# Kernel tuning notes

Hardware: AMD Instinct MI355X
Metric: run time of the kernel (lower is better)

The kernel has to match this reference:

```python
import jax, jax.numpy as jnp
import numpy as np

EPS = 1e-08

def log_g(x):
    return jnp.log(jnp.tanh(x) + EPS)

def parallel_scan(log_coeffs, log_values):
    # log_coeffs: [B, L, H], log_values: [B, L+1, H]
    a_star = jnp.pad(jnp.cumsum(log_coeffs, axis=1), ((0, 0), (1, 0), (0, 0)))
    log_h0_plus_b_star = jax.lax.cumlogsumexp(log_values - a_star, axis=1)
    log_h = a_star + log_h0_plus_b_star
    return jnp.exp(log_h)[:, 1:, :]

def setup_inputs() -> dict:
    key = jax.random.key(0)
    B, L, I, H, O = 16, 4096, 64, 512, 1
    ks = jax.random.split(key, 8)
    s_i = 1.0 / np.sqrt(I)
    s_h = 1.0 / np.sqrt(H)
    return {
        "x": jax.random.normal(ks[0], (B, L, I), dtype=jnp.float32),
        "Wz0": jax.random.uniform(ks[1], (I, H), jnp.float32, -s_i, s_i),
        "bz0": jnp.zeros((H,), jnp.float32),
        "Wh0": jax.random.uniform(ks[2], (I, H), jnp.float32, -s_i, s_i),
        "bh0": jnp.zeros((H,), jnp.float32),
        "Wz1": jax.random.uniform(ks[3], (H, H), jnp.float32, -s_h, s_h),
        "bz1": jnp.zeros((H,), jnp.float32),
        "Wh1": jax.random.uniform(ks[4], (H, H), jnp.float32, -s_h, s_h),
        "bh1": jnp.zeros((H,), jnp.float32),
        "Wf": jax.random.uniform(ks[5], (H, O), jnp.float32, -s_h, s_h),
        "bf": jnp.zeros((O,), jnp.float32),
    }

def min_gru_layer(inp, Wz, bz, Wh, bh):
    B, L, _ = inp.shape
    H = Wz.shape[1]
    k = jax.nn.sigmoid(inp @ Wz + bz)          # [B, L, H]
    log_z = -jax.nn.softplus(-k)               # (faithful: softplus of sigmoid output)
    log_coeffs = -jax.nn.softplus(k)
    log_h0 = jnp.full((B, 1, H), jnp.log(EPS), dtype=inp.dtype)  # log_g(zeros)
    log_h_wavy = log_g(jax.nn.sigmoid(inp @ Wh + bh))
    log_values = jnp.concatenate([log_h0, log_z + log_h_wavy], axis=1)  # [B, L+1, H]
    return parallel_scan(log_coeffs, log_values)

def reference(x, Wz0, bz0, Wh0, bh0, Wz1, bz1, Wh1, bh1, Wf, bf):
    h = min_gru_layer(x, Wz0, bz0, Wh0, bh0)
    h = min_gru_layer(h, Wz1, bz1, Wh1, bh1)
    return h[:, -1, :] @ Wf + bf  # [B, output_size]
```

## Files before the change

### kernel.cpp

```cpp
#include <hip/hip_runtime.h>
#include <hip/hip_fp16.h>

#define EPSF 1e-8f

typedef _Float16 half8 __attribute__((ext_vector_type(8)));
typedef float f32x4 __attribute__((ext_vector_type(4)));


__device__ __forceinline__ float fast_rcp(float x) {
    return __builtin_amdgcn_rcpf(x);
}
__device__ __forceinline__ void gate_transform(float pz, float ph, float& a, float& b) {
    float ez = __expf(-pz);
    float k  = fast_rcp(1.0f + ez);
    float ek = __expf(-k);
    float z  = fast_rcp(1.0f + ek);
    a = ek * z;
    float es = __expf(-ph);
    float s  = fast_rcp(1.0f + es);
    float e2 = __expf(-2.0f * s);
    float hw = (1.0f - e2) * fast_rcp(1.0f + e2) + EPSF;
    b = z * hw;
}

__device__ __forceinline__ void gload16(const void* g, void* l) {
    __builtin_amdgcn_global_load_lds(
        (const __attribute__((address_space(1))) unsigned int*)g,
        (__attribute__((address_space(3))) unsigned int*)l, 16, 0, 0);
}

__device__ __forceinline__ void qscan(int q, float pA, float pB,
                                      float& fA, float& fB, float& prA, float& prB)
{
    float oA = __shfl_xor(pA, 16, 64), oB = __shfl_xor(pB, 16, 64);
    float eA = (q & 1) ? oA : pA, eB = (q & 1) ? oB : pB;
    float lA = (q & 1) ? pA : oA, lB = (q & 1) ? pB : oB;
    float p2A = eA * lA;
    float p2B = fmaf(lA, eB, lB);
    float o2A = __shfl_xor(p2A, 32, 64), o2B = __shfl_xor(p2B, 32, 64);
    float loA = (q & 2) ? o2A : p2A, loB = (q & 2) ? o2B : p2B;
    float hiA = (q & 2) ? p2A : o2A, hiB = (q & 2) ? p2B : o2B;
    fA = loA * hiA;
    fB = fmaf(hiA, loB, hiB);
    prA = (q & 2) ? o2A : 1.0f;
    prB = (q & 2) ? o2B : 0.0f;
    if (q & 1) { prB = fmaf(oA, prB, oB); prA *= oA; }
}

__global__ __launch_bounds__(256) void k1s(
    const float* __restrict__ x,
    const float* __restrict__ Wz0, const float* __restrict__ Wh0,
    const float* __restrict__ Wz1, const float* __restrict__ Wh1,
    const float* __restrict__ bz, const float* __restrict__ bh,
    const float* __restrict__ bf,
    __half* __restrict__ Wtz1, __half* __restrict__ Wth1,
    __half* __restrict__ h0red, float* __restrict__ out)
{
    __shared__ char smem1[49408];
    __half* As = (__half*)smem1;
    __half* Bs = As + 128 * 64;
    float (*t)[65] = (float(*)[65])(smem1 + 32768);
    float* carray = (float*)(smem1 + 16384);
    __half* h0s = (__half*)smem1;
    const int tid = threadIdx.x;
    const int wave = tid >> 6, lane = tid & 63;
    const int q = lane >> 4, l16 = lane & 15;
    const int wm = wave >> 1, wn = wave & 1;

    const int bx = blockIdx.x, by = blockIdx.y;
    const int Lb = bx + 8 * by;
    const int n0 = bx * 64;
    const float* xsrc = x + (size_t)by * 262144 + 253952;

    if (Lb == 0 && tid < 16) out[tid] = bf[0];

    {
        const int r8 = lane >> 3, ch = lane & 7;
#pragma unroll
        for (int i = 0; i < 4; ++i) {
            const int reg = wave * 4 + i;
            const int row = reg * 8 + r8;
            const int c0 = (ch ^ (row & 7)) * 8;
            float4 v0 = *(const float4*)(xsrc + row * 64 + c0);
            float4 v1 = *(const float4*)(xsrc + row * 64 + c0 + 4);
            __half2* dst = (__half2*)((char*)As + reg * 1024 + lane * 16);
            dst[0] = __floats2half2_rn(v0.x, v0.y);
            dst[1] = __floats2half2_rn(v0.z, v0.w);
            dst[2] = __floats2half2_rn(v1.x, v1.y);
            dst[3] = __floats2half2_rn(v1.z, v1.w);
        }
    }

    const int r = tid >> 4, c4 = (tid & 15) * 4;
    {
        const int mat = Lb >> 6, ti = Lb & 63;
        const int n0t = (ti & 7) * 64, k0t = (ti >> 3) * 64;
        const float* W = mat ? Wh1 : Wz1;
        __half* Wt = mat ? Wth1 : Wtz1;
#pragma unroll
        for (int rr = 0; rr < 64; rr += 16)
            *(float4*)&t[rr + r][c4] = *(const float4*)&W[(size_t)(k0t + rr + r) * 512 + n0t + c4];
        __syncthreads();
#pragma unroll
        for (int rr = 0; rr < 64; rr += 16) {
            const int row = rr + r;
            __half2 h01 = __floats2half2_rn(t[c4 + 0][row], t[c4 + 1][row]);
            __half2 h23 = __floats2half2_rn(t[c4 + 2][row], t[c4 + 3][row]);
            *(__half2*)&Wt[(size_t)(n0t + row) * 512 + k0t + c4] = h01;
            *(__half2*)&Wt[(size_t)(n0t + row) * 512 + k0t + c4 + 2] = h23;
        }
    }
    {
        const int n = tid & 63, cw = (tid >> 6) * 2;
#pragma unroll
        for (int mat = 0; mat < 2; ++mat) {
            const float* W = mat ? Wh0 : Wz0;
            __syncthreads();
#pragma unroll
            for (int rr = 0; rr < 64; rr += 16)
                *(float4*)&t[rr + r][c4] = *(const float4*)&W[(size_t)(rr + r) * 512 + n0 + c4];
            __syncthreads();
#pragma unroll
            for (int cc = 0; cc < 2; ++cc) {
                const int chunk = cw + cc;
                half8 hv;
#pragma unroll
                for (int j = 0; j < 8; ++j) hv[j] = (_Float16)t[chunk * 8 + j][n];
                *(half8*)&Bs[(mat * 64 + n) * 64 + ((chunk ^ (n & 7)) << 3)] = hv;
            }
        }
    }
    __syncthreads();

    f32x4 accz[4][2], acch[4][2];
#pragma unroll
    for (int mi = 0; mi < 4; ++mi)
#pragma unroll
        for (int ni = 0; ni < 2; ++ni) {
            accz[mi][ni] = (f32x4){0.f, 0.f, 0.f, 0.f};
            acch[mi][ni] = (f32x4){0.f, 0.f, 0.f, 0.f};
        }

#pragma unroll
    for (int s = 0; s < 2; ++s) {
        half8 af[4];
#pragma unroll
        for (int mi = 0; mi < 4; ++mi) {
            const int row = wm * 64 + mi * 16 + l16;
            const int pc = (s * 4 + q) ^ (row & 7);
            af[mi] = *(const half8*)&As[row * 64 + pc * 8];
        }
#pragma unroll
        for (int ni = 0; ni < 2; ++ni) {
            const int rn = wn * 32 + ni * 16 + l16;
            const int pc = (s * 4 + q) ^ (rn & 7);
            half8 bzf = *(const half8*)&Bs[rn * 64 + pc * 8];
            half8 bhf = *(const half8*)&Bs[(64 + rn) * 64 + pc * 8];
#pragma unroll
            for (int mi = 0; mi < 4; ++mi) {
                accz[mi][ni] = __builtin_amdgcn_mfma_f32_16x16x32_f16(af[mi], bzf, accz[mi][ni], 0, 0, 0);
                acch[mi][ni] = __builtin_amdgcn_mfma_f32_16x16x32_f16(af[mi], bhf, acch[mi][ni], 0, 0, 0);
            }
        }
    }

    float rB[2];
    if (wm == 0) {
#pragma unroll
        for (int ni = 0; ni < 2; ++ni) {
            const int col = n0 + wn * 32 + ni * 16 + l16;
            const float bzv = bz[col], bhv = bh[col];
            float runA = 1.f, runB = 0.f;
#pragma unroll
            for (int mi = 0; mi < 4; ++mi) {
                float av[4], bv[4], pA = 1.f, pB = 0.f;
#pragma unroll
                for (int j = 0; j < 4; ++j) {
                    gate_transform(accz[mi][ni][j] + bzv, acch[mi][ni][j] + bhv, av[j], bv[j]);
                    pB = fmaf(av[j], pB, bv[j]); pA *= av[j];
                }
                float fA, fB, prA, prB;
                qscan(q, pA, pB, fA, fB, prA, prB);
                runB = fmaf(fA, runB, fB); runA *= fA;
            }
            rB[ni] = runB;
        }
    }
    __syncthreads();
    if (wm == 0 && q == 0) {
#pragma unroll
        for (int ni = 0; ni < 2; ++ni)
            carray[wn * 32 + ni * 16 + l16] = rB[ni];
    }
    __syncthreads();
    if (wm == 1) {
#pragma unroll
        for (int ni = 0; ni < 2; ++ni) {
            const int colloc = wn * 32 + ni * 16 + l16;
            const int col = n0 + colloc;
            const float bzv = bz[col], bhv = bh[col];
            float H = carray[colloc];
#pragma unroll
            for (int mi = 0; mi < 4; ++mi) {
                float av[4], bv[4], pA = 1.f, pB = 0.f;
#pragma unroll
                for (int j = 0; j < 4; ++j) {
                    gate_transform(accz[mi][ni][j] + bzv, acch[mi][ni][j] + bhv, av[j], bv[j]);
                    pB = fmaf(av[j], pB, bv[j]); pA *= av[j];
                }
                float fA, fB, prA, prB;
                qscan(q, pA, pB, fA, fB, prA, prB);
                float Hl = fmaf(prA, H, prB);
                const int rloc = mi * 16 + q * 4;
#pragma unroll
                for (int j = 0; j < 4; ++j) {
                    Hl = fmaf(av[j], Hl, bv[j]);
                    h0s[(rloc + j) * 68 + colloc] = (__half)Hl;
                }
                H = fmaf(fA, H, fB);
            }
        }
    }
    __syncthreads();
    {
        const int row = tid >> 2, cpart = tid & 3;
        const __half* srcp = h0s + row * 68 + cpart * 16;
        __half* dstp = h0red + (size_t)(by * 64 + row) * 512 + n0 + cpart * 16;
        *(uint4*)dstp = *(const uint4*)srcp;
        *(uint4*)(dstp + 8) = *(const uint4*)(srcp + 8);
    }
}

__global__ __launch_bounds__(256, 2) void k4_l1(
    const __half* __restrict__ h0red,
    const __half* __restrict__ Wtz, const __half* __restrict__ Wth,
    const float* __restrict__ bz, const float* __restrict__ bh,
    const float* __restrict__ Wf, float* __restrict__ out)
{
    __shared__ char smem4[2][24576];
    const int tid = threadIdx.x;
    const int wave = tid >> 6, lane = tid & 63;
    const int q = lane >> 4, l16 = lane & 15;
    const int wm = wave >> 1, wn = wave & 1;

    const int bx = blockIdx.x, by = blockIdx.y;
    const int m0 = by * 128, n0 = bx * 128;

    const int r4 = lane >> 2, ch = lane & 3;

    const __half* aSrc[2]; int aDst[2];
#pragma unroll
    for (int i = 0; i < 2; ++i) {
        const int reg = wave * 2 + i;
        const int row = reg * 16 + r4;
        const int pc = ch ^ ((row >> 1) & 3);
        aSrc[i] = h0red + (size_t)(m0 + row) * 512 + pc * 8;
        aDst[i] = reg * 1024;
    }
    const __half* bSrc[4]; int bDst[4];
#pragma unroll
    for (int i = 0; i < 4; ++i) {
        const int reg = wave * 4 + i;
        const int row = reg * 16 + r4;
        const int pc = ch ^ ((row >> 1) & 3);
        bSrc[i] = ((row < 128) ? (Wtz + (size_t)(n0 + row) * 512)
                               : (Wth + (size_t)(n0 + row - 128) * 512)) + pc * 8;
        bDst[i] = 8192 + reg * 1024;
    }
    int aOff[4], bOff[4];
#pragma unroll
    for (int mi = 0; mi < 4; ++mi) {
        const int row = wm * 64 + mi * 16 + l16;
        aOff[mi] = row * 64 + ((q ^ ((row >> 1) & 3)) << 4);
    }
#pragma unroll
    for (int ni = 0; ni < 4; ++ni) {
        const int rn = wn * 64 + ni * 16 + l16;
        bOff[ni] = 8192 + rn * 64 + ((q ^ ((rn >> 1) & 3)) << 4);
    }

    f32x4 accz[4][4], acch[4][4];
#pragma unroll
    for (int mi = 0; mi < 4; ++mi)
#pragma unroll
        for (int ni = 0; ni < 4; ++ni) {
            accz[mi][ni] = (f32x4){0.f, 0.f, 0.f, 0.f};
            acch[mi][ni] = (f32x4){0.f, 0.f, 0.f, 0.f};
        }

    auto stage = [&](int c, int t) {
#pragma unroll
        for (int i = 0; i < 2; ++i)
            gload16(aSrc[i] + t * 32, smem4[c] + aDst[i]);
#pragma unroll
        for (int i = 0; i < 4; ++i)
            gload16(bSrc[i] + t * 32, smem4[c] + bDst[i]);
    };
    auto compute = [&](int c) {
        half8 af[4];
#pragma unroll
        for (int mi = 0; mi < 4; ++mi)
            af[mi] = *(const half8*)(smem4[c] + aOff[mi]);
        __builtin_amdgcn_s_setprio(1);
#pragma unroll
        for (int ni = 0; ni < 4; ++ni) {
            half8 bzf = *(const half8*)(smem4[c] + bOff[ni]);
            half8 bhf = *(const half8*)(smem4[c] + 8192 + bOff[ni]);
#pragma unroll
            for (int mi = 0; mi < 4; ++mi) {
                accz[mi][ni] = __builtin_amdgcn_mfma_f32_16x16x32_f16(af[mi], bzf, accz[mi][ni], 0, 0, 0);
                acch[mi][ni] = __builtin_amdgcn_mfma_f32_16x16x32_f16(af[mi], bhf, acch[mi][ni], 0, 0, 0);
            }
        }
        __builtin_amdgcn_s_setprio(0);
    };

    stage(0, 0);
#pragma unroll
    for (int t = 0; t < 15; ++t) {
        const int c = t & 1;
        stage(c ^ 1, t + 1);
        asm volatile("s_waitcnt vmcnt(6)" ::: "memory");
        __builtin_amdgcn_s_barrier();
        compute(c);
        __builtin_amdgcn_s_barrier();
    }
    asm volatile("s_waitcnt vmcnt(0)" ::: "memory");
    __builtin_amdgcn_s_barrier();
    compute(1);

    const int batch = by * 2 + wm;
    float part = 0.f;
#pragma unroll
    for (int ni = 0; ni < 4; ++ni) {
        const int col = n0 + wn * 64 + ni * 16 + l16;
        const float bzv = bz[col], bhv = bh[col];
        float fullA = 1.f, fullB = 0.f;
#pragma unroll
        for (int mi = 0; mi < 4; ++mi) {
            float pA = 1.f, pB = 0.f;
#pragma unroll
            for (int j = 0; j < 4; ++j) {
                float a, b;
                gate_transform(accz[mi][ni][j] + bzv, acch[mi][ni][j] + bhv, a, b);
                pB = fmaf(a, pB, b); pA *= a;
            }
            float fA, fB, prA, prB;
            qscan(q, pA, pB, fA, fB, prA, prB);
            fullB = fmaf(fA, fullB, fB); fullA *= fA;
        }
        if (q == 0) part = fmaf(fullB, Wf[col], part);
    }
#pragma unroll
    for (int off = 32; off; off >>= 1) part += __shfl_down(part, off, 64);
    if (lane == 0) atomicAdd(&out[batch], part);
}

extern "C" void kernel_launch(void* const* d_in, const int* in_sizes, int n_in,
                              void* d_out, int out_size, void* d_ws, size_t ws_size,
                              hipStream_t stream)
{
    const float* x   = (const float*)d_in[0];
    const float* Wz0 = (const float*)d_in[1];
    const float* bz0 = (const float*)d_in[2];
    const float* Wh0 = (const float*)d_in[3];
    const float* bh0 = (const float*)d_in[4];
    const float* Wz1 = (const float*)d_in[5];
    const float* bz1 = (const float*)d_in[6];
    const float* Wh1 = (const float*)d_in[7];
    const float* bh1 = (const float*)d_in[8];
    const float* Wf  = (const float*)d_in[9];
    const float* bf  = (const float*)d_in[10];
    float* out = (float*)d_out;

    char* ws = (char*)d_ws;
    __half* h0red = (__half*)ws;
    __half* Wtz1  = (__half*)(ws + (1024 << 10));
    __half* Wth1  = Wtz1 + 262144;

    k1s<<<dim3(8, 16), 256, 0, stream>>>(x, Wz0, Wh0, Wz1, Wh1, bz0, bh0, bf,
                                         Wtz1, Wth1, h0red, out);
    k4_l1<<<dim3(4, 8), 256, 0, stream>>>(h0red, Wtz1, Wth1, bz1, bh1, Wf, out);
}
```

Baseline: 32.31 us.

## Fuse both layer kernels into one launch with a global atomic barrier

Merges the layer-0 kernel and the layer-1 GEMM/scan kernel into a single 128-block launch. After writing its layer-0 hidden states, each block bumps a global counter. The first 32 blocks spin until all 128 have arrived, then run the layer-1 work. This removes one kernel launch gap but adds a memset before the launch, spin-wait latency, and reliance on all 128 blocks being co-resident so the barrier cannot deadlock.

Measured after the change: 42.62 us. 31.9% more time.

```diff
diff --git a/kernel.cpp b/kernel.cpp
--- a/kernel.cpp
+++ b/kernel.cpp
@@ -47,313 +47,320 @@
     if (q & 1) { prB = fmaf(oA, prB, oB); prA *= oA; }
 }
 
-__global__ __launch_bounds__(256) void k1s(
+__global__ __launch_bounds__(256) void kfused(
     const float* __restrict__ x,
     const float* __restrict__ Wz0, const float* __restrict__ Wh0,
     const float* __restrict__ Wz1, const float* __restrict__ Wh1,
-    const float* __restrict__ bz, const float* __restrict__ bh,
-    const float* __restrict__ bf,
+    const float* __restrict__ bz0, const float* __restrict__ bh0,
+    const float* __restrict__ bz1, const float* __restrict__ bh1,
+    const float* __restrict__ Wf, const float* __restrict__ bf,
     __half* __restrict__ Wtz1, __half* __restrict__ Wth1,
-    __half* __restrict__ h0red, float* __restrict__ out)
+    __half* __restrict__ h0red, unsigned int* __restrict__ cnt,
+    float* __restrict__ out)
 {
-    __shared__ char smem1[49408];
-    __half* As = (__half*)smem1;
-    __half* Bs = As + 128 * 64;
-    float (*t)[65] = (float(*)[65])(smem1 + 32768);
-    float* carray = (float*)(smem1 + 16384);
-    __half* h0s = (__half*)smem1;
+    __shared__ char smem[49408];
     const int tid = threadIdx.x;
     const int wave = tid >> 6, lane = tid & 63;
     const int q = lane >> 4, l16 = lane & 15;
     const int wm = wave >> 1, wn = wave & 1;
-
-    const int bx = blockIdx.x, by = blockIdx.y;
-    const int Lb = bx + 8 * by;
-    const int n0 = bx * 64;
-    const float* xsrc = x + (size_t)by * 262144 + 253952;
-
-    if (Lb == 0 && tid < 16) out[tid] = bf[0];
+    const int Lb = blockIdx.x;
 
     {
-        const int r8 = lane >> 3, ch = lane & 7;
+        __half* As = (__half*)smem;
+        __half* Bs = As + 128 * 64;
+        float (*t)[65] = (float(*)[65])(smem + 32768);
+        float* carray = (float*)(smem + 16384);
+        __half* h0s = (__half*)smem;
+
+        const int bx = Lb & 7, by = Lb >> 3;
+        const int n0 = bx * 64;
+        const float* xsrc = x + (size_t)by * 262144 + 253952;
+
+        if (Lb == 0 && tid < 16) out[tid] = bf[0];
+
+        {
+            const int r8 = lane >> 3, ch = lane & 7;
+#pragma unroll
+            for (int i = 0; i < 4; ++i) {
+                const int reg = wave * 4 + i;
+                const int row = reg * 8 + r8;
+                const int c0 = (ch ^ (row & 7)) * 8;
+                float4 v0 = *(const float4*)(xsrc + row * 64 + c0);
+                float4 v1 = *(const float4*)(xsrc + row * 64 + c0 + 4);
+                __half2* dst = (__half2*)((char*)As + reg * 1024 + lane * 16);
+                dst[0] = __floats2half2_rn(v0.x, v0.y);
+                dst[1] = __floats2half2_rn(v0.z, v0.w);
+                dst[2] = __floats2half2_rn(v1.x, v1.y);
+                dst[3] = __floats2half2_rn(v1.z, v1.w);
+            }
+        }
+
+        const int r = tid >> 4, c4 = (tid & 15) * 4;
+        {
+            const int mat = Lb >> 6, ti = Lb & 63;
+            const int n0t = (ti & 7) * 64, k0t = (ti >> 3) * 64;
+            const float* W = mat ? Wh1 : Wz1;
+            __half* Wt = mat ? Wth1 : Wtz1;
+#pragma unroll
+            for (int rr = 0; rr < 64; rr += 16)
+                *(float4*)&t[rr + r][c4] = *(const float4*)&W[(size_t)(k0t + rr + r) * 512 + n0t + c4];
+            __syncthreads();
+#pragma unroll
+            for (int rr = 0; rr < 64; rr += 16) {
+                const int row = rr + r;
+                __half2 h01 = __floats2half2_rn(t[c4 + 0][row], t[c4 + 1][row]);
+                __half2 h23 = __floats2half2_rn(t[c4 + 2][row], t[c4 + 3][row]);
+                *(__half2*)&Wt[(size_t)(n0t + row) * 512 + k0t + c4] = h01;
+                *(__half2*)&Wt[(size_t)(n0t + row) * 512 + k0t + c4 + 2] = h23;
+            }
+        }
+        {
+            const int n = tid & 63, cw = (tid >> 6) * 2;
+#pragma unroll
+            for (int mat = 0; mat < 2; ++mat) {
+                const float* W = mat ? Wh0 : Wz0;
+                __syncthreads();
+#pragma unroll
+                for (int rr = 0; rr < 64; rr += 16)
+                    *(float4*)&t[rr + r][c4] = *(const float4*)&W[(size_t)(rr + r) * 512 + n0 + c4];
+                __syncthreads();
+#pragma unroll
+                for (int cc = 0; cc < 2; ++cc) {
+                    const int chunk = cw + cc;
+                    half8 hv;
+#pragma unroll
+                    for (int j = 0; j < 8; ++j) hv[j] = (_Float16)t[chunk * 8 + j][n];
+                    *(half8*)&Bs[(mat * 64 + n) * 64 + ((chunk ^ (n & 7)) << 3)] = hv;
+                }
+            }
+        }
+        __syncthreads();
+
+        f32x4 accz[4][2], acch[4][2];
+#pragma unroll
+        for (int mi = 0; mi < 4; ++mi)
+#pragma unroll
+            for (int ni = 0; ni < 2; ++ni) {
+                accz[mi][ni] = (f32x4){0.f, 0.f, 0.f, 0.f};
+                acch[mi][ni] = (f32x4){0.f, 0.f, 0.f, 0.f};
+            }
+
+#pragma unroll
+        for (int s = 0; s < 2; ++s) {
+            half8 af[4];
+#pragma unroll
+            for (int mi = 0; mi < 4; ++mi) {
+                const int row = wm * 64 + mi * 16 + l16;
+                const int pc = (s * 4 + q) ^ (row & 7);
+                af[mi] = *(const half8*)&As[row * 64 + pc * 8];
+            }
+#pragma unroll
+            for (int ni = 0; ni < 2; ++ni) {
+                const int rn = wn * 32 + ni * 16 + l16;
+                const int pc = (s * 4 + q) ^ (rn & 7);
+                half8 bzf = *(const half8*)&Bs[rn * 64 + pc * 8];
+                half8 bhf = *(const half8*)&Bs[(64 + rn) * 64 + pc * 8];
+#pragma unroll
+                for (int mi = 0; mi < 4; ++mi) {
+                    accz[mi][ni] = __builtin_amdgcn_mfma_f32_16x16x32_f16(af[mi], bzf, accz[mi][ni], 0, 0, 0);
+                    acch[mi][ni] = __builtin_amdgcn_mfma_f32_16x16x32_f16(af[mi], bhf, acch[mi][ni], 0, 0, 0);
+                }
+            }
+        }
+
+        float rB[2];
+        if (wm == 0) {
+#pragma unroll
+            for (int ni = 0; ni < 2; ++ni) {
+                const int col = n0 + wn * 32 + ni * 16 + l16;
+                const float bzv = bz0[col], bhv = bh0[col];
+                float runA = 1.f, runB = 0.f;
+#pragma unroll
+                for (int mi = 0; mi < 4; ++mi) {
+                    float av[4], bv[4], pA = 1.f, pB = 0.f;
+#pragma unroll
+                    for (int j = 0; j < 4; ++j) {
+                        gate_transform(accz[mi][ni][j] + bzv, acch[mi][ni][j] + bhv, av[j], bv[j]);
+                        pB = fmaf(av[j], pB, bv[j]); pA *= av[j];
+                    }
+                    float fA, fB, prA, prB;
+                    qscan(q, pA, pB, fA, fB, prA, prB);
+                    runB = fmaf(fA, runB, fB); runA *= fA;
+                }
+                rB[ni] = runB;
+            }
+        }
+        __syncthreads();
+        if (wm == 0 && q == 0) {
+#pragma unroll
+            for (int ni = 0; ni < 2; ++ni)
+                carray[wn * 32 + ni * 16 + l16] = rB[ni];
+        }
+        __syncthreads();
+        if (wm == 1) {
+#pragma unroll
+            for (int ni = 0; ni < 2; ++ni) {
+                const int colloc = wn * 32 + ni * 16 + l16;
+                const int col = n0 + colloc;
+                const float bzv = bz0[col], bhv = bh0[col];
+                float H = carray[colloc];
+#pragma unroll
+                for (int mi = 0; mi < 4; ++mi) {
+                    float av[4], bv[4], pA = 1.f, pB = 0.f;
+#pragma unroll
+                    for (int j = 0; j < 4; ++j) {
+                        gate_transform(accz[mi][ni][j] + bzv, acch[mi][ni][j] + bhv, av[j], bv[j]);
+                        pB = fmaf(av[j], pB, bv[j]); pA *= av[j];
+                    }
+                    float fA, fB, prA, prB;
+                    qscan(q, pA, pB, fA, fB, prA, prB);
+                    float Hl = fmaf(prA, H, prB);
+                    const int rloc = mi * 16 + q * 4;
+#pragma unroll
+                    for (int j = 0; j < 4; ++j) {
+                        Hl = fmaf(av[j], Hl, bv[j]);
+                        h0s[(rloc + j) * 68 + colloc] = (__half)Hl;
+                    }
+                    H = fmaf(fA, H, fB);
+                }
+            }
+        }
+        __syncthreads();
+        {
+            const int row = tid >> 2, cpart = tid & 3;
+            const __half* srcp = h0s + row * 68 + cpart * 16;
+            __half* dstp = h0red + (size_t)(by * 64 + row) * 512 + n0 + cpart * 16;
+            *(uint4*)dstp = *(const uint4*)srcp;
+            *(uint4*)(dstp + 8) = *(const uint4*)(srcp + 8);
+        }
+    }
+
+    __syncthreads();
+    if (tid == 0) {
+        __threadfence();
+        atomicAdd(cnt, 1u);
+    }
+    if (Lb >= 32) return;
+    if (tid == 0) {
+        while (__hip_atomic_load(cnt, __ATOMIC_RELAXED, __HIP_MEMORY_SCOPE_AGENT) < 128u)
+            __builtin_amdgcn_s_sleep(2);
+    }
+    __syncthreads();
+    __threadfence();
+
+    {
+        char* smem4 = smem;
+        const int bx = Lb & 3, by = Lb >> 2;
+        const int m0 = by * 128, n0 = bx * 128;
+        const int r4 = lane >> 2, ch = lane & 3;
+
+        const __half* aSrc[2]; int aDst[2];
+#pragma unroll
+        for (int i = 0; i < 2; ++i) {
+            const int reg = wave * 2 + i;
+            const int row = reg * 16 + r4;
+            const int pc = ch ^ ((row >> 1) & 3);
+            aSrc[i] = h0red + (size_t)(m0 + row) * 512 + pc * 8;
+            aDst[i] = reg * 1024;
+        }
+        const __half* bSrc[4]; int bDst[4];
 #pragma unroll
         for (int i = 0; i < 4; ++i) {
             const int reg = wave * 4 + i;
-            const int row = reg * 8 + r8;
-            const int c0 = (ch ^ (row & 7)) * 8;
-            float4 v0 = *(const float4*)(xsrc + row * 64 + c0);
-            float4 v1 = *(const float4*)(xsrc + row * 64 + c0 + 4);
-            __half2* dst = (__half2*)((char*)As + reg * 1024 + lane * 16);
-            dst[0] = __floats2half2_rn(v0.x, v0.y);
-            dst[1] = __floats2half2_rn(v0.z, v0.w);
-            dst[2] = __floats2half2_rn(v1.x, v1.y);
-            dst[3] = __floats2half2_rn(v1.z, v1.w);
-        }
-    }
-
-    const int r = tid >> 4, c4 = (tid & 15) * 4;
-    {
-        const int mat = Lb >> 6, ti = Lb & 63;
-        const int n0t = (ti & 7) * 64, k0t = (ti >> 3) * 64;
-        const float* W = mat ? Wh1 : Wz1;
-        __half* Wt = mat ? Wth1 : Wtz1;
-#pragma unroll
-        for (int rr = 0; rr < 64; rr += 16)
-            *(float4*)&t[rr + r][c4] = *(const float4*)&W[(size_t)(k0t + rr + r) * 512 + n0t + c4];
-        __syncthreads();
-#pragma unroll
-        for (int rr = 0; rr < 64; rr += 16) {
-            const int row = rr + r;
-            __half2 h01 = __floats2half2_rn(t[c4 + 0][row], t[c4 + 1][row]);
-            __half2 h23 = __floats2half2_rn(t[c4 + 2][row], t[c4 + 3][row]);
-            *(__half2*)&Wt[(size_t)(n0t + row) * 512 + k0t + c4] = h01;
-            *(__half2*)&Wt[(size_t)(n0t + row) * 512 + k0t + c4 + 2] = h23;
-        }
-    }
-    {
-        const int n = tid & 63, cw = (tid >> 6) * 2;
-#pragma unroll
-        for (int mat = 0; mat < 2; ++mat) {
-            const float* W = mat ? Wh0 : Wz0;
-            __syncthreads();
-#pragma unroll
-            for (int rr = 0; rr < 64; rr += 16)
-                *(float4*)&t[rr + r][c4] = *(const float4*)&W[(size_t)(rr + r) * 512 + n0 + c4];
-            __syncthreads();
-#pragma unroll
-            for (int cc = 0; cc < 2; ++cc) {
-                const int chunk = cw + cc;
-                half8 hv;
-#pragma unroll
-                for (int j = 0; j < 8; ++j) hv[j] = (_Float16)t[chunk * 8 + j][n];
-                *(half8*)&Bs[(mat * 64 + n) * 64 + ((chunk ^ (n & 7)) << 3)] = hv;
-            }
-        }
-    }
-    __syncthreads();
-
-    f32x4 accz[4][2], acch[4][2];
-#pragma unroll
-    for (int mi = 0; mi < 4; ++mi)
-#pragma unroll
-        for (int ni = 0; ni < 2; ++ni) {
-            accz[mi][ni] = (f32x4){0.f, 0.f, 0.f, 0.f};
-            acch[mi][ni] = (f32x4){0.f, 0.f, 0.f, 0.f};
-        }
-
-#pragma unroll
-    for (int s = 0; s < 2; ++s) {
-        half8 af[4];
+            const int row = reg * 16 + r4;
+            const int pc = ch ^ ((row >> 1) & 3);
+            bSrc[i] = ((row < 128) ? (Wtz1 + (size_t)(n0 + row) * 512)
+                                   : (Wth1 + (size_t)(n0 + row - 128) * 512)) + pc * 8;
+            bDst[i] = 8192 + reg * 1024;
+        }
+        int aOff[4], bOff[4];
 #pragma unroll
         for (int mi = 0; mi < 4; ++mi) {
             const int row = wm * 64 + mi * 16 + l16;
-            const int pc = (s * 4 + q) ^ (row & 7);
-            af[mi] = *(const half8*)&As[row * 64 + pc * 8];
-        }
-#pragma unroll
-        for (int ni = 0; ni < 2; ++ni) {
-            const int rn = wn * 32 + ni * 16 + l16;
-            const int pc = (s * 4 + q) ^ (rn & 7);
-            half8 bzf = *(const half8*)&Bs[rn * 64 + pc * 8];
-            half8 bhf = *(const half8*)&Bs[(64 + rn) * 64 + pc * 8];
+            aOff[mi] = row * 64 + ((q ^ ((row >> 1) & 3)) << 4);
+        }
+#pragma unroll
+        for (int ni = 0; ni < 4; ++ni) {
+            const int rn = wn * 64 + ni * 16 + l16;
+            bOff[ni] = 8192 + rn * 64 + ((q ^ ((rn >> 1) & 3)) << 4);
+        }
+
+        f32x4 accz[4][4], acch[4][4];
+#pragma unroll
+        for (int mi = 0; mi < 4; ++mi)
+#pragma unroll
+            for (int ni = 0; ni < 4; ++ni) {
+                accz[mi][ni] = (f32x4){0.f, 0.f, 0.f, 0.f};
+                acch[mi][ni] = (f32x4){0.f, 0.f, 0.f, 0.f};
+            }
+
+        auto stage = [&](int c, int t) {
+#pragma unroll
+            for (int i = 0; i < 2; ++i)
+                gload16(aSrc[i] + t * 32, smem4 + c * 24576 + aDst[i]);
+#pragma unroll
+            for (int i = 0; i < 4; ++i)
+                gload16(bSrc[i] + t * 32, smem4 + c * 24576 + bDst[i]);
+        };
+        auto compute = [&](int c) {
+            half8 af[4];
+#pragma unroll
+            for (int mi = 0; mi < 4; ++mi)
+                af[mi] = *(const half8*)(smem4 + c * 24576 + aOff[mi]);
+            __builtin_amdgcn_s_setprio(1);
+#pragma unroll
+            for (int ni = 0; ni < 4; ++ni) {
+                half8 bzf = *(const half8*)(smem4 + c * 24576 + bOff[ni]);
+                half8 bhf = *(const half8*)(smem4 + c * 24576 + 8192 + bOff[ni]);
+#pragma unroll
+                for (int mi = 0; mi < 4; ++mi) {
+                    accz[mi][ni] = __builtin_amdgcn_mfma_f32_16x16x32_f16(af[mi], bzf, accz[mi][ni], 0, 0, 0);
+                    acch[mi][ni] = __builtin_amdgcn_mfma_f32_16x16x32_f16(af[mi], bhf, acch[mi][ni], 0, 0, 0);
+                }
+            }
+            __builtin_amdgcn_s_setprio(0);
+        };
+
+        stage(0, 0);
+#pragma unroll
+        for (int t = 0; t < 15; ++t) {
+            const int c = t & 1;
+            stage(c ^ 1, t + 1);
+            asm volatile("s_waitcnt vmcnt(6)" ::: "memory");
+            __builtin_amdgcn_s_barrier();
+            compute(c);
+            __builtin_amdgcn_s_barrier();
+        }
+        asm volatile("s_waitcnt vmcnt(0)" ::: "memory");
+        __builtin_amdgcn_s_barrier();
+        compute(1);
+
+        const int batch = by * 2 + wm;
+        float part = 0.f;
+#pragma unroll
+        for (int ni = 0; ni < 4; ++ni) {
+            const int col = n0 + wn * 64 + ni * 16 + l16;
+            const float bzv = bz1[col], bhv = bh1[col];
+            float fullA = 1.f, fullB = 0.f;
 #pragma unroll
             for (int mi = 0; mi < 4; ++mi) {
-                accz[mi][ni] = __builtin_amdgcn_mfma_f32_16x16x32_f16(af[mi], bzf, accz[mi][ni], 0, 0, 0);
-                acch[mi][ni] = __builtin_amdgcn_mfma_f32_16x16x32_f16(af[mi], bhf, acch[mi][ni], 0, 0, 0);
-            }
-        }
-    }
-
-    float rB[2];
-    if (wm == 0) {
-#pragma unroll
-        for (int ni = 0; ni < 2; ++ni) {
-            const int col = n0 + wn * 32 + ni * 16 + l16;
-            const float bzv = bz[col], bhv = bh[col];
-            float runA = 1.f, runB = 0.f;
-#pragma unroll
-            for (int mi = 0; mi < 4; ++mi) {
-                float av[4], bv[4], pA = 1.f, pB = 0.f;
+                float pA = 1.f, pB = 0.f;
 #pragma unroll
                 for (int j = 0; j < 4; ++j) {
-                    gate_transform(accz[mi][ni][j] + bzv, acch[mi][ni][j] + bhv, av[j], bv[j]);
-                    pB = fmaf(av[j], pB, bv[j]); pA *= av[j];
+                    float a, b;
+                    gate_transform(accz[mi][ni][j] + bzv, acch[mi][ni][j] + bhv, a, b);
+                    pB = fmaf(a, pB, b); pA *= a;
                 }
                 float fA, fB, prA, prB;
                 qscan(q, pA, pB, fA, fB, prA, prB);
-                runB = fmaf(fA, runB, fB); runA *= fA;
-            }
-            rB[ni] = runB;
-        }
+                fullB = fmaf(fA, fullB, fB); fullA *= fA;
+            }
+            if (q == 0) part = fmaf(fullB, Wf[col], part);
+        }
+#pragma unroll
+        for (int off = 32; off; off >>= 1) part += __shfl_down(part, off, 64);
+        if (lane == 0) atomicAdd(&out[batch], part);
     }
-    __syncthreads();
-    if (wm == 0 && q == 0) {
-#pragma unroll
-        for (int ni = 0; ni < 2; ++ni)
-            carray[wn * 32 + ni * 16 + l16] = rB[ni];
-    }
-    __syncthreads();
-    if (wm == 1) {
-#pragma unroll
-        for (int ni = 0; ni < 2; ++ni) {
-            const int colloc = wn * 32 + ni * 16 + l16;
-            const int col = n0 + colloc;
-            const float bzv = bz[col], bhv = bh[col];
-            float H = carray[colloc];
-#pragma unroll
-            for (int mi = 0; mi < 4; ++mi) {
-                float av[4], bv[4], pA = 1.f, pB = 0.f;
-#pragma unroll
-                for (int j = 0; j < 4; ++j) {
-                    gate_transform(accz[mi][ni][j] + bzv, acch[mi][ni][j] + bhv, av[j], bv[j]);
-                    pB = fmaf(av[j], pB, bv[j]); pA *= av[j];
-                }
-                float fA, fB, prA, prB;
-                qscan(q, pA, pB, fA, fB, prA, prB);
-                float Hl = fmaf(prA, H, prB);
-                const int rloc = mi * 16 + q * 4;
-#pragma unroll
-                for (int j = 0; j < 4; ++j) {
-                    Hl = fmaf(av[j], Hl, bv[j]);
-                    h0s[(rloc + j) * 68 + colloc] = (__half)Hl;
-                }
-                H = fmaf(fA, H, fB);
-            }
-        }
-    }
-    __syncthreads();
-    {
-        const int row = tid >> 2, cpart = tid & 3;
-        const __half* srcp = h0s + row * 68 + cpart * 16;
-        __half* dstp = h0red + (size_t)(by * 64 + row) * 512 + n0 + cpart * 16;
-        *(uint4*)dstp = *(const uint4*)srcp;
-        *(uint4*)(dstp + 8) = *(const uint4*)(srcp + 8);
-    }
-}
-
-__global__ __launch_bounds__(256, 2) void k4_l1(
-    const __half* __restrict__ h0red,
-    const __half* __restrict__ Wtz, const __half* __restrict__ Wth,
-    const float* __restrict__ bz, const float* __restrict__ bh,
-    const float* __restrict__ Wf, float* __restrict__ out)
-{
-    __shared__ char smem4[2][24576];
-    const int tid = threadIdx.x;
-    const int wave = tid >> 6, lane = tid & 63;
-    const int q = lane >> 4, l16 = lane & 15;
-    const int wm = wave >> 1, wn = wave & 1;
-
-    const int bx = blockIdx.x, by = blockIdx.y;
-    const int m0 = by * 128, n0 = bx * 128;
-
-    const int r4 = lane >> 2, ch = lane & 3;
-
-    const __half* aSrc[2]; int aDst[2];
-#pragma unroll
-    for (int i = 0; i < 2; ++i) {
-        const int reg = wave * 2 + i;
-        const int row = reg * 16 + r4;
-        const int pc = ch ^ ((row >> 1) & 3);
-        aSrc[i] = h0red + (size_t)(m0 + row) * 512 + pc * 8;
-        aDst[i] = reg * 1024;
-    }
-    const __half* bSrc[4]; int bDst[4];
-#pragma unroll
-    for (int i = 0; i < 4; ++i) {
-        const int reg = wave * 4 + i;
-        const int row = reg * 16 + r4;
-        const int pc = ch ^ ((row >> 1) & 3);
-        bSrc[i] = ((row < 128) ? (Wtz + (size_t)(n0 + row) * 512)
-                               : (Wth + (size_t)(n0 + row - 128) * 512)) + pc * 8;
-        bDst[i] = 8192 + reg * 1024;
-    }
-    int aOff[4], bOff[4];
-#pragma unroll
-    for (int mi = 0; mi < 4; ++mi) {
-        const int row = wm * 64 + mi * 16 + l16;
-        aOff[mi] = row * 64 + ((q ^ ((row >> 1) & 3)) << 4);
-    }
-#pragma unroll
-    for (int ni = 0; ni < 4; ++ni) {
-        const int rn = wn * 64 + ni * 16 + l16;
-        bOff[ni] = 8192 + rn * 64 + ((q ^ ((rn >> 1) & 3)) << 4);
-    }
-
-    f32x4 accz[4][4], acch[4][4];
-#pragma unroll
-    for (int mi = 0; mi < 4; ++mi)
-#pragma unroll
-        for (int ni = 0; ni < 4; ++ni) {
-            accz[mi][ni] = (f32x4){0.f, 0.f, 0.f, 0.f};
-            acch[mi][ni] = (f32x4){0.f, 0.f, 0.f, 0.f};
-        }
-
-    auto stage = [&](int c, int t) {
-#pragma unroll
-        for (int i = 0; i < 2; ++i)
-            gload16(aSrc[i] + t * 32, smem4[c] + aDst[i]);
-#pragma unroll
-        for (int i = 0; i < 4; ++i)
-            gload16(bSrc[i] + t * 32, smem4[c] + bDst[i]);
-    };
-    auto compute = [&](int c) {
-        half8 af[4];
-#pragma unroll
-        for (int mi = 0; mi < 4; ++mi)
-            af[mi] = *(const half8*)(smem4[c] + aOff[mi]);
-        __builtin_amdgcn_s_setprio(1);
-#pragma unroll
-        for (int ni = 0; ni < 4; ++ni) {
-            half8 bzf = *(const half8*)(smem4[c] + bOff[ni]);
-            half8 bhf = *(const half8*)(smem4[c] + 8192 + bOff[ni]);
-#pragma unroll
-            for (int mi = 0; mi < 4; ++mi) {
-                accz[mi][ni] = __builtin_amdgcn_mfma_f32_16x16x32_f16(af[mi], bzf, accz[mi][ni], 0, 0, 0);
-                acch[mi][ni] = __builtin_amdgcn_mfma_f32_16x16x32_f16(af[mi], bhf, acch[mi][ni], 0, 0, 0);
-            }
-        }
-        __builtin_amdgcn_s_setprio(0);
-    };
-
-    stage(0, 0);
-#pragma unroll
-    for (int t = 0; t < 15; ++t) {
-        const int c = t & 1;
-        stage(c ^ 1, t + 1);
-        asm volatile("s_waitcnt vmcnt(6)" ::: "memory");
-        __builtin_amdgcn_s_barrier();
-        compute(c);
-        __builtin_amdgcn_s_barrier();
-    }
-    asm volatile("s_waitcnt vmcnt(0)" ::: "memory");
-    __builtin_amdgcn_s_barrier();
-    compute(1);
-
-    const int batch = by * 2 + wm;
-    float part = 0.f;
-#pragma unroll
-    for (int ni = 0; ni < 4; ++ni) {
-        const int col = n0 + wn * 64 + ni * 16 + l16;
-        const float bzv = bz[col], bhv = bh[col];
-        float fullA = 1.f, fullB = 0.f;
-#pragma unroll
-        for (int mi = 0; mi < 4; ++mi) {
-            float pA = 1.f, pB = 0.f;
-#pragma unroll
-            for (int j = 0; j < 4; ++j) {
-                float a, b;
-                gate_transform(accz[mi][ni][j] + bzv, acch[mi][ni][j] + bhv, a, b);
-                pB = fmaf(a, pB, b); pA *= a;
-            }
-            float fA, fB, prA, prB;
-            qscan(q, pA, pB, fA, fB, prA, prB);
-            fullB = fmaf(fA, fullB, fB); fullA *= fA;
-        }
-        if (q == 0) part = fmaf(fullB, Wf[col], part);
-    }
-#pragma unroll
-    for (int off = 32; off; off >>= 1) part += __shfl_down(part, off, 64);
-    if (lane == 0) atomicAdd(&out[batch], part);
 }
 
 extern "C" void kernel_launch(void* const* d_in, const int* in_sizes, int n_in,
@@ -377,8 +384,9 @@
     __half* h0red = (__half*)ws;
     __half* Wtz1  = (__half*)(ws + (1024 << 10));
     __half* Wth1  = Wtz1 + 262144;
-
-    k1s<<<dim3(8, 16), 256, 0, stream>>>(x, Wz0, Wh0, Wz1, Wh1, bz0, bh0, bf,
-                                         Wtz1, Wth1, h0red, out);
-    k4_l1<<<dim3(4, 8), 256, 0, stream>>>(h0red, Wtz1, Wth1, bz1, bh1, Wf, out);
-}
+    unsigned int* cnt = (unsigned int*)(ws + (2048 << 10));
+
+    hipMemsetAsync(cnt, 0, sizeof(unsigned int), stream);
+    kfused<<<128, 256, 0, stream>>>(x, Wz0, Wh0, Wz1, Wh1, bz0, bh0, bz1, bh1,
+                                    Wf, bf, Wtz1, Wth1, h0red, cnt, out);
+}
```
